# Kernel tuning notes

Measured on AMD Instinct MI355X. Metric: run time of the kernel, lower is better.

The kernel has to match this reference:

```python
import jax, jax.numpy as jnp
import numpy as np

B, S, D, H, E = 4, 1024, 1024, 16, 4
HD = D // H
FF = 4 * D
EPS = 1e-5


def _ln(x):
    # normalize only; per-expert affine applied by caller
    mu = jnp.mean(x, axis=-1, keepdims=True)
    var = jnp.mean(jnp.square(x - mu), axis=-1, keepdims=True)
    return (x - mu) * jax.lax.rsqrt(var + EPS)


def setup_inputs() -> dict:
    key = jax.random.key(0)
    ks = jax.random.split(key, 12)
    s = 0.02
    inp = {
        "x": jax.random.normal(ks[0], (B, S, D), jnp.float32),
        # attention router
        "Wr_a": jax.random.normal(ks[1], (D, E), jnp.float32) * s,
        "br_a": jnp.zeros((E,), jnp.float32),
        # per-expert attention params
        "g_a": jnp.ones((E, D), jnp.float32),
        "b_a": jnp.zeros((E, D), jnp.float32),
        "Wqkv": jax.random.normal(ks[2], (E, D, 3 * D), jnp.float32) * s,
        "bqkv": jnp.zeros((E, 3 * D), jnp.float32),
        "Wpr": jax.random.normal(ks[3], (E, D, D), jnp.float32) * s,
        "bpr": jnp.zeros((E, D), jnp.float32),
        # MLP router
        "Wr_m": jax.random.normal(ks[4], (D, E), jnp.float32) * s,
        "br_m": jnp.zeros((E,), jnp.float32),
        # per-expert MLP params
        "g_m": jnp.ones((E, D), jnp.float32),
        "b_m": jnp.zeros((E, D), jnp.float32),
        "Wfc": jax.random.normal(ks[5], (E, D, FF), jnp.float32) * s,
        "bfc": jnp.zeros((E, FF), jnp.float32),
        "Wp2": jax.random.normal(ks[6], (E, FF, D), jnp.float32) * s,
        "bp2": jnp.zeros((E, D), jnp.float32),
    }
    return inp


def _block(x, Wr_a, br_a, g_a, b_a, Wqkv, bqkv, Wpr, bpr,
           Wr_m, br_m, g_m, b_m, Wfc, bfc, Wp2, bp2):
    N = B * S
    h = x.reshape(N, D)

    # ---- MoT attention (routing_all_possible_path: dense score-weighted mix) ----
    score = jax.nn.softmax(h @ Wr_a + br_a, axis=-1)          # [N,E]
    hn = _ln(h)                                                # shared normalization
    hln = hn[None, :, :] * g_a[:, None, :] + b_a[:, None, :]  # [E,N,D]
    qkv_e = jnp.einsum('end,edf->enf', hln, Wqkv) + bqkv[:, None, :]  # [E,N,3D]
    qkv = jnp.einsum('ne,enf->nf', score, qkv_e)               # [N,3D]

    q, k, v = jnp.split(qkv.reshape(B, S, 3 * D), 3, axis=-1)
    q = q.reshape(B, S, H, HD).transpose(0, 2, 1, 3)           # [B,H,S,hd]
    k = k.reshape(B, S, H, HD).transpose(0, 2, 1, 3)
    v = v.reshape(B, S, H, HD).transpose(0, 2, 1, 3)

    aw = jnp.einsum('bhqd,bhkd->bhqk', q, k) / jnp.sqrt(jnp.float32(HD))
    causal = jnp.tril(jnp.ones((S, S), bool))
    aw = jnp.where(causal, aw, jnp.finfo(aw.dtype).min)
    p = jax.nn.softmax(aw, axis=-1)
    a = jnp.einsum('bhqk,bhkd->bhqd', p, v)                    # [B,H,S,hd]
    a = a.transpose(0, 2, 1, 3).reshape(N, D)

    attn_out = jnp.einsum('ne,nd,edf->nf', score, a, Wpr) + score @ bpr
    y = x + attn_out.reshape(B, S, D)

    # ---- MoT MLP (same dense routed-expert pattern) ----
    h2 = y.reshape(N, D)
    score2 = jax.nn.softmax(h2 @ Wr_m + br_m, axis=-1)         # [N,E]
    hn2 = _ln(h2)
    hln2 = hn2[None, :, :] * g_m[:, None, :] + b_m[:, None, :]  # [E,N,D]
    inter = jax.nn.gelu(jnp.einsum('end,edf->enf', hln2, Wfc) + bfc[:, None, :])  # [E,N,FF]
    mlp_out = jnp.einsum('ne,enf,efd->nd', score2, inter, Wp2) + score2 @ bp2
    return y + mlp_out.reshape(B, S, D)


def reference(x, Wr_a, br_a, g_a, b_a, Wqkv, bqkv, Wpr, bpr,
              Wr_m, br_m, g_m, b_m, Wfc, bfc, Wp2, bp2):
    return _block(x, Wr_a, br_a, g_a, b_a, Wqkv, bqkv, Wpr, bpr,
                  Wr_m, br_m, g_m, b_m, Wfc, bfc, Wp2, bp2)
```

## Files before the change

kernel.cpp:

```cpp
#include <hip/hip_runtime.h>
#include <hip/hip_bf16.h>

typedef __bf16 bf16x8 __attribute__((ext_vector_type(8)));
typedef float f32x4 __attribute__((ext_vector_type(4)));
typedef unsigned short u16;
typedef u16 u16x8 __attribute__((ext_vector_type(8)));

#define B_ 4
#define S_ 1024
#define D_ 1024
#define E_ 4
#define H_ 16
#define FF_ 4096
#define N_ 4096

__device__ __forceinline__ u16 f2bf(float f) {
  __hip_bfloat16 h = __float2bfloat16(f);
  return *reinterpret_cast<u16*>(&h);
}
__device__ __forceinline__ float bf2f(u16 v) {
  return __uint_as_float(((unsigned)v) << 16);
}

#define BAR()                         \
  {                                   \
    asm volatile("" ::: "memory");    \
    __builtin_amdgcn_s_barrier();     \
    asm volatile("" ::: "memory");    \
  }

__global__ __launch_bounds__(256) void tcvt(const float* __restrict__ src,
                                            u16* __restrict__ dst, int R, int C) {
  __shared__ float t[32][33];
  int r0 = blockIdx.y * 32, c0 = blockIdx.x * 32;
  int tx = threadIdx.x, ty = threadIdx.y;
#pragma unroll
  for (int i = 0; i < 4; i++)
    t[ty + i * 8][tx] = src[(long)(r0 + ty + i * 8) * C + c0 + tx];
  __syncthreads();
#pragma unroll
  for (int i = 0; i < 4; i++)
    dst[(long)(c0 + ty + i * 8) * R + r0 + tx] = f2bf(t[tx][ty + i * 8]);
}

template <int YMODE>
__global__ __launch_bounds__(256) void ln_router_expand(
    const float* __restrict__ X, const float* __restrict__ Wr, const float* __restrict__ br,
    const float* __restrict__ g, const float* __restrict__ bb,
    float* __restrict__ score_out, u16* __restrict__ Aout,
    long stride_e, long stride_n, int scale_flag,
    const float* __restrict__ score_a, const float* __restrict__ bpr,
    const u16* __restrict__ prt, float* __restrict__ ybuf) {
  int n = blockIdx.x, t = threadIdx.x;
  int lane = t & 63, wave = t >> 6;
  const float* xr = X + (long)n * D_;
  float xv[4];
  float vals[6] = {0.f, 0.f, 0.f, 0.f, 0.f, 0.f};
  float4 sa4;
  if (YMODE) sa4 = reinterpret_cast<const float4*>(score_a)[n];
#pragma unroll
  for (int i = 0; i < 4; i++) {
    int d = i * 256 + t;
    float v = xr[d];
    if (YMODE) {
      long idx = (long)n * D_ + d;
      v += sa4.x * bpr[d] + sa4.y * bpr[D_ + d] + sa4.z * bpr[2 * D_ + d] +
           sa4.w * bpr[3 * D_ + d];
#pragma unroll
      for (int zz = 0; zz < 4; zz++) v += bf2f(prt[(long)zz * 4194304 + idx]);
      ybuf[idx] = v;
    }
    xv[i] = v;
    vals[0] += v;
    vals[1] += v * v;
    float4 w = reinterpret_cast<const float4*>(Wr)[d];
    vals[2] += v * w.x; vals[3] += v * w.y; vals[4] += v * w.z; vals[5] += v * w.w;
  }
#pragma unroll
  for (int o = 1; o < 64; o <<= 1) {
#pragma unroll
    for (int j = 0; j < 6; j++) vals[j] += __shfl_xor(vals[j], o, 64);
  }
  __shared__ float red[4][6];
  if (lane == 0) {
#pragma unroll
    for (int j = 0; j < 6; j++) red[wave][j] = vals[j];
  }
  __syncthreads();
  float tot[6];
#pragma unroll
  for (int j = 0; j < 6; j++) tot[j] = red[0][j] + red[1][j] + red[2][j] + red[3][j];
  float mean = tot[0] * (1.0f / D_);
  float var = tot[1] * (1.0f / D_) - mean * mean;
  float rstd = rsqrtf(var + 1e-5f);
  float lg0 = tot[2] + br[0], lg1 = tot[3] + br[1], lg2 = tot[4] + br[2], lg3 = tot[5] + br[3];
  float mx = fmaxf(fmaxf(lg0, lg1), fmaxf(lg2, lg3));
  float e0 = __expf(lg0 - mx), e1 = __expf(lg1 - mx), e2 = __expf(lg2 - mx), e3 = __expf(lg3 - mx);
  float inv = 1.0f / (e0 + e1 + e2 + e3);
  float sc[4] = {e0 * inv, e1 * inv, e2 * inv, e3 * inv};
  if (t == 0) {
    float4 s4 = make_float4(sc[0], sc[1], sc[2], sc[3]);
    *reinterpret_cast<float4*>(&score_out[(long)n * 4]) = s4;
  }
#pragma unroll
  for (int i = 0; i < 4; i++) {
    int d = i * 256 + t;
    float hn = (xv[i] - mean) * rstd;
#pragma unroll
    for (int e = 0; e < 4; e++) {
      float val = hn * g[e * D_ + d] + bb[e * D_ + d];
      if (scale_flag) val *= sc[e];
      Aout[(long)e * stride_e + (long)n * stride_n + d] = f2bf(val);
    }
  }
}

template <int MODE>
__global__ __launch_bounds__(512, 2) void g8(
    const u16* __restrict__ A, const u16* __restrict__ Bt, int K, int N, int kslice,
    const float* __restrict__ score, const float* __restrict__ bias,
    u16* __restrict__ outb, int eidx, long zstride) {
  __shared__ __align__(16) u16 lds0[65536];
  const int tid = threadIdx.x;
  const int w = tid >> 6, lane = tid & 63;
  const int l15 = lane & 15, l4 = lane >> 4;
  const int wr = w >> 2, wc = w & 3;

  const int gx = gridDim.x, gy = gridDim.y;
  const int total = gx * gy * gridDim.z;
  const int flat = blockIdx.x + gx * (blockIdx.y + gy * blockIdx.z);
  const int cpx = total >> 3;
  const int nf = (flat & 7) * cpx + (flat >> 3);
  const int bxi = nf % gx;
  const int tmp = nf / gx;
  const int byi = tmp % gy;
  const int z = tmp / gy;

  const long bm = (long)byi * 256, bn = (long)bxi * 256;
  const long k0 = (long)z * kslice;
  const int nt = kslice >> 6;

  const int cp = lane & 3;
  const int sr0 = w * 32 + (lane >> 2);
  const int sr1 = sr0 + 16;
  const int cl0 = cp ^ ((sr0 >> 1) & 3);
  const int cl1 = cp ^ ((sr1 >> 1) & 3);
  const u16* gA0 = A + (bm + sr0) * (long)K + k0 + cl0 * 8;
  const u16* gA1 = A + (bm + sr1) * (long)K + k0 + cl1 * 8;
  const u16* gB0 = Bt + (bn + sr0) * (long)K + k0 + cl0 * 8;
  const u16* gB1 = Bt + (bn + sr1) * (long)K + k0 + cl1 * 8;
  const int e0 = w * 1024;
  const int e1 = w * 1024 + 512;

  const int chA = l4 ^ ((l15 >> 1) & 3);
  const int rdA = (wr * 128 + l15) * 32 + chA * 8;
  const int rdB = (wc * 64 + l15) * 32 + chA * 8;

#define GLD(gsrc, ldsoff)                                                              \
  __builtin_amdgcn_global_load_lds(                                                    \
      (const __attribute__((address_space(1))) void*)(gsrc),                           \
      (__attribute__((address_space(3))) void*)(lds0 + (ldsoff)), 16, 0, 0)

  GLD(gA0, 0 + e0);
  GLD(gA1, 0 + e1);
  GLD(gB0, 16384 + e0);
  GLD(gB1, 16384 + e1);
  GLD(gA0 + 32, 8192 + e0);
  GLD(gA1 + 32, 8192 + e1);
  GLD(gB0 + 32, 24576 + e0);
  GLD(gB1 + 32, 24576 + e1);
  if (nt > 1) {
    GLD(gA0 + 64, 32768 + e0);
    GLD(gA1 + 64, 32768 + e1);
    GLD(gB0 + 64, 32768 + 16384 + e0);
    GLD(gB1 + 64, 32768 + 16384 + e1);
    asm volatile("s_waitcnt vmcnt(8)" ::: "memory");
  } else {
    asm volatile("s_waitcnt vmcnt(4)" ::: "memory");
  }
  BAR();

  f32x4 acc[8][4] = {};
  bf16x8 a[4], b[4];

  for (int t = 0; t < nt; ++t) {
    const int base = (t & 1) * 32768;
    const int nb = base ^ 32768;
    const long ko1 = (long)(t + 1) * 64 + 32;
    const long ko2 = (long)(t + 2) * 64;
#pragma unroll
    for (int i = 0; i < 4; i++) a[i] = *(const bf16x8*)(lds0 + base + rdA + i * 512);
#pragma unroll
    for (int i = 0; i < 4; i++) b[i] = *(const bf16x8*)(lds0 + base + 16384 + rdB + i * 512);
    if (t + 1 < nt) {
      GLD(gA0 + ko1, nb + 8192 + e0);
      GLD(gA1 + ko1, nb + 8192 + e1);
    }
    BAR();
    __builtin_amdgcn_s_setprio(1);
#pragma unroll
    for (int mi = 0; mi < 4; mi++)
#pragma unroll
      for (int ni = 0; ni < 4; ni++)
        acc[mi][ni] = __builtin_amdgcn_mfma_f32_16x16x32_bf16(a[mi], b[ni], acc[mi][ni], 0, 0, 0);
    __builtin_amdgcn_s_setprio(0);
    BAR();
#pragma unroll
    for (int i = 0; i < 4; i++) a[i] = *(const bf16x8*)(lds0 + base + rdA + (4 + i) * 512);
    if (t + 1 < nt) {
      GLD(gB0 + ko1, nb + 24576 + e0);
      GLD(gB1 + ko1, nb + 24576 + e1);
    }
    BAR();
    __builtin_amdgcn_s_setprio(1);
#pragma unroll
    for (int mi = 0; mi < 4; mi++)
#pragma unroll
      for (int ni = 0; ni < 4; ni++)
        acc[4 + mi][ni] =
            __builtin_amdgcn_mfma_f32_16x16x32_bf16(a[mi], b[ni], acc[4 + mi][ni], 0, 0, 0);
    __builtin_amdgcn_s_setprio(0);
    if (t + 1 < nt) {
      asm volatile("s_waitcnt vmcnt(8)" ::: "memory");
    } else {
      asm volatile("s_waitcnt vmcnt(0)" ::: "memory");
    }
    BAR();
#pragma unroll
    for (int i = 0; i < 4; i++) a[i] = *(const bf16x8*)(lds0 + base + 8192 + rdA + i * 512);
#pragma unroll
    for (int i = 0; i < 4; i++) b[i] = *(const bf16x8*)(lds0 + base + 24576 + rdB + i * 512);
    if (t + 2 < nt) {
      GLD(gA0 + ko2, base + e0);
      GLD(gA1 + ko2, base + e1);
    }
    BAR();
    __builtin_amdgcn_s_setprio(1);
#pragma unroll
    for (int mi = 0; mi < 4; mi++)
#pragma unroll
      for (int ni = 0; ni < 4; ni++)
        acc[mi][ni] = __builtin_amdgcn_mfma_f32_16x16x32_bf16(a[mi], b[ni], acc[mi][ni], 0, 0, 0);
    __builtin_amdgcn_s_setprio(0);
    BAR();
#pragma unroll
    for (int i = 0; i < 4; i++)
      a[i] = *(const bf16x8*)(lds0 + base + 8192 + rdA + (4 + i) * 512);
    if (t + 2 < nt) {
      GLD(gB0 + ko2, base + 16384 + e0);
      GLD(gB1 + ko2, base + 16384 + e1);
    }
    BAR();
    __builtin_amdgcn_s_setprio(1);
#pragma unroll
    for (int mi = 0; mi < 4; mi++)
#pragma unroll
      for (int ni = 0; ni < 4; ni++)
        acc[4 + mi][ni] =
            __builtin_amdgcn_mfma_f32_16x16x32_bf16(a[mi], b[ni], acc[4 + mi][ni], 0, 0, 0);
    __builtin_amdgcn_s_setprio(0);
    if (t + 2 < nt) {
      asm volatile("s_waitcnt vmcnt(8)" ::: "memory");
    } else if (t + 1 < nt) {
      asm volatile("s_waitcnt vmcnt(4)" ::: "memory");
    } else {
      asm volatile("s_waitcnt vmcnt(0)" ::: "memory");
    }
    BAR();
  }
#undef GLD

  const long zoff = (long)z * zstride;
#pragma unroll
  for (int ni = 0; ni < 4; ni++) {
    long col = bn + wc * 64 + ni * 16 + l15;
    float b4[4];
    float bcol = 0.0f;
    if (MODE == 0) {
#pragma unroll
      for (int e = 0; e < 4; e++) b4[e] = bias[(long)e * N + col];
    } else if (MODE == 2) {
      bcol = bias[col];
    }
#pragma unroll
    for (int mi = 0; mi < 8; mi++) {
#pragma unroll
      for (int r = 0; r < 4; r++) {
        long row = bm + wr * 128 + mi * 16 + l4 * 4 + r;
        float v = acc[mi][ni][r];
        if (MODE == 0) {
          float4 s4 = reinterpret_cast<const float4*>(score)[row];
          v += s4.x * b4[0] + s4.y * b4[1] + s4.z * b4[2] + s4.w * b4[3];
          outb[row * (long)N + col] = f2bf(v);
        } else if (MODE == 2) {
          float u = v + bcol;
          float zz = 0.7978845608f * (u + 0.044715f * u * u * u);
          float tt = __expf(2.0f * zz);
          float gel = u * (1.0f - 1.0f / (tt + 1.0f));
          outb[row * (long)N + col] = f2bf(gel * score[row * 4 + eidx]);
        } else {
          outb[zoff + row * (long)N + col] = f2bf(v);
        }
      }
    }
  }
}

__global__ __launch_bounds__(256) void attn_kernel(const u16* __restrict__ qkv,
                                                   const float* __restrict__ score_a,
                                                   u16* __restrict__ A_pr) {
  __shared__ __align__(16) u16 Kt[32 * 64];
  __shared__ __align__(16) u16 VT[64 * 32];
  __shared__ __align__(16) u16 Pl[4][16 * 32];
  int tid = threadIdx.x, wave = tid >> 6, lane = tid & 63;
  int l15 = lane & 15, l4 = lane >> 4;
  int qblk = blockIdx.x, bh = blockIdx.y;
  int b = bh >> 4, h = bh & 15;
  int q0 = qblk * 64 + wave * 16;
  const long LD = 3072;

  bf16x8 qf[2];
  {
    const u16* qp = qkv + (long)(b * 1024 + q0 + l15) * LD + h * 64 + l4 * 8;
    qf[0] = *(const bf16x8*)qp;
    qf[1] = *(const bf16x8*)(qp + 32);
  }
  f32x4 acc[4] = {};
  float m_run = -1e30f, l_run = 0.0f;
  int kv_end = qblk * 64 + 64;

  for (int kv0 = 0; kv0 < kv_end; kv0 += 32) {
    {
      int r = tid >> 3, c = (tid & 7) * 8;
      const u16* kp = qkv + (long)(b * 1024 + kv0 + r) * LD + 1024 + h * 64 + c;
      *(u16x8*)&Kt[r * 64 + c] = *(const u16x8*)kp;
      u16x8 vv = *(const u16x8*)(kp + 1024);
#pragma unroll
      for (int j = 0; j < 8; j++) VT[(c + j) * 32 + r] = vv[j];
    }
    __syncthreads();
    if (kv0 < q0 + 16) {
      float p[8];
      float pmax = -1e30f;
      int qg = q0 + l15;
#pragma unroll
      for (int ks = 0; ks < 2; ks++) {
        f32x4 st = {};
#pragma unroll
        for (int kc = 0; kc < 2; kc++) {
          bf16x8 kf = *(const bf16x8*)&Kt[(ks * 16 + l15) * 64 + kc * 32 + l4 * 8];
          st = __builtin_amdgcn_mfma_f32_16x16x32_bf16(kf, qf[kc], st, 0, 0, 0);
        }
#pragma unroll
        for (int r = 0; r < 4; r++) {
          int kvg = kv0 + ks * 16 + l4 * 4 + r;
          float v = st[r] * 0.125f;
          if (kvg > qg) v = -1e30f;
          p[ks * 4 + r] = v;
          pmax = fmaxf(pmax, v);
        }
      }
      pmax = fmaxf(pmax, __shfl_xor(pmax, 16, 64));
      pmax = fmaxf(pmax, __shfl_xor(pmax, 32, 64));
      float m_new = fmaxf(m_run, pmax);
      float alpha = __expf(m_run - m_new);
      float rsum = 0.f;
#pragma unroll
      for (int i = 0; i < 8; i++) {
        p[i] = __expf(p[i] - m_new);
        rsum += p[i];
      }
      rsum += __shfl_xor(rsum, 16, 64);
      rsum += __shfl_xor(rsum, 32, 64);
      l_run = l_run * alpha + rsum;
      m_run = m_new;
      float af4[4];
#pragma unroll
      for (int r = 0; r < 4; r++) af4[r] = __shfl(alpha, l4 * 4 + r, 64);
#pragma unroll
      for (int i = 0; i < 4; i++) {
#pragma unroll
        for (int r = 0; r < 4; r++) acc[i][r] *= af4[r];
      }
      u16* pw = &Pl[wave][0];
#pragma unroll
      for (int i = 0; i < 8; i++) {
        int ks = i >> 2, r = i & 3;
        pw[l15 * 32 + ks * 16 + l4 * 4 + r] = f2bf(p[i]);
      }
      bf16x8 pa = *(const bf16x8*)&pw[l15 * 32 + l4 * 8];
#pragma unroll
      for (int i = 0; i < 4; i++) {
        bf16x8 vf = *(const bf16x8*)&VT[(i * 16 + l15) * 32 + l4 * 8];
        acc[i] = __builtin_amdgcn_mfma_f32_16x16x32_bf16(pa, vf, acc[i], 0, 0, 0);
      }
    }
    __syncthreads();
  }

  float linv[4];
#pragma unroll
  for (int r = 0; r < 4; r++) {
    float lv = __shfl(l_run, l4 * 4 + r, 64);
    linv[r] = 1.0f / lv;
  }
#pragma unroll
  for (int r = 0; r < 4; r++) {
    int q = l4 * 4 + r;
    long nrow = (long)b * 1024 + q0 + q;
    float4 s4 = reinterpret_cast<const float4*>(score_a)[nrow];
    float se[4] = {s4.x, s4.y, s4.z, s4.w};
#pragma unroll
    for (int i = 0; i < 4; i++) {
      float v = acc[i][r] * linv[r];
      int d = h * 64 + i * 16 + l15;
#pragma unroll
      for (int e = 0; e < 4; e++) A_pr[nrow * 4096 + e * 1024 + d] = f2bf(se[e] * v);
    }
  }
}

template <int FIRST>
__global__ __launch_bounds__(256) void accum_out(const float* __restrict__ ybuf,
                                                 const float* __restrict__ score_m,
                                                 const float* __restrict__ bp2,
                                                 const u16* __restrict__ p2t,
                                                 float* __restrict__ out) {
  int n = blockIdx.x, t = threadIdx.x;
#pragma unroll
  for (int i = 0; i < 4; i++) {
    int d = i * 256 + t;
    long idx = (long)n * D_ + d;
    float v;
    if (FIRST) {
      float4 s4 = reinterpret_cast<const float4*>(score_m)[n];
      v = ybuf[idx] + s4.x * bp2[d] + s4.y * bp2[D_ + d] + s4.z * bp2[2 * D_ + d] +
          s4.w * bp2[3 * D_ + d];
    } else {
      v = out[idx];
    }
#pragma unroll
    for (int zz = 0; zz < 4; zz++) v += bf2f(p2t[(long)zz * 4194304 + idx]);
    out[idx] = v;
  }
}

extern "C" void kernel_launch(void* const* d_in, const int* in_sizes, int n_in, void* d_out,
                              int out_size, void* d_ws, size_t ws_size, hipStream_t stream) {
  (void)in_sizes; (void)n_in; (void)out_size; (void)ws_size;
  const float* x    = (const float*)d_in[0];
  const float* Wr_a = (const float*)d_in[1];
  const float* br_a = (const float*)d_in[2];
  const float* g_a  = (const float*)d_in[3];
  const float* b_a  = (const float*)d_in[4];
  const float* Wqkv = (const float*)d_in[5];
  const float* bqkv = (const float*)d_in[6];
  const float* Wpr  = (const float*)d_in[7];
  const float* bpr  = (const float*)d_in[8];
  const float* Wr_m = (const float*)d_in[9];
  const float* br_m = (const float*)d_in[10];
  const float* g_m  = (const float*)d_in[11];
  const float* b_m  = (const float*)d_in[12];
  const float* Wfc  = (const float*)d_in[13];
  const float* bfc  = (const float*)d_in[14];
  const float* Wp2  = (const float*)d_in[15];
  const float* bp2  = (const float*)d_in[16];
  float* out = (float*)d_out;

  char* ws = (char*)d_ws;
  const size_t oW = 0;
  const size_t oA = 25165824;
  const size_t oQ = oA + 33554432;
  const size_t oP = oQ + 33554432;
  const size_t oY = oP + 33554432;
  const size_t oS = oY + 16777216;
  u16* wt_qkv  = (u16*)(ws + oW);
  u16* wt_pr   = (u16*)(ws + oW);
  u16* wt_fce  = (u16*)(ws + oW);
  u16* wt_p2e  = (u16*)(ws + oW + (size_t)8 * 1024 * 1024);
  u16* A_a     = (u16*)(ws + oA);
  u16* prt     = (u16*)(ws + oA);
  u16* A_fc    = (u16*)(ws + oA);
  u16* qkvb    = (u16*)(ws + oQ);
  u16* p2t     = (u16*)(ws + oQ);
  u16* A_pr    = (u16*)(ws + oP);
  u16* inter   = (u16*)(ws + oP);
  float* ybuf  = (float*)(ws + oY);
  float* score_a = (float*)(ws + oS);
  float* score_m = (float*)(ws + oS + 65536);

  dim3 tb(32, 8);
  tcvt<<<dim3(3072 / 32, 4096 / 32), tb, 0, stream>>>(Wqkv, wt_qkv, 4096, 3072);
  ln_router_expand<0><<<N_, 256, 0, stream>>>(x, Wr_a, br_a, g_a, b_a, score_a, A_a,
                                              (long)1024, (long)4096, 1,
                                              nullptr, nullptr, nullptr, nullptr);
  g8<0><<<dim3(3072 / 256, 4096 / 256, 1), 512, 0, stream>>>(
      A_a, wt_qkv, 4096, 3072, 4096, score_a, bqkv, qkvb, 0, 0L);
  attn_kernel<<<dim3(S_ / 64, B_ * H_), 256, 0, stream>>>(qkvb, score_a, A_pr);
  tcvt<<<dim3(1024 / 32, 4096 / 32), tb, 0, stream>>>(Wpr, wt_pr, 4096, 1024);
  g8<4><<<dim3(1024 / 256, 4096 / 256, 4), 512, 0, stream>>>(
      A_pr, wt_pr, 4096, 1024, 1024, nullptr, nullptr, prt, 0, (long)4096 * 1024);

  ln_router_expand<1><<<N_, 256, 0, stream>>>(x, Wr_m, br_m, g_m, b_m,
                                              score_m, A_fc, (long)N_ * 1024, (long)1024, 0,
                                              score_a, bpr, prt, ybuf);
  for (int e = 0; e < 4; e++) {
    tcvt<<<dim3(4096 / 32, 1024 / 32), tb, 0, stream>>>(
        Wfc + (size_t)e * 1024 * 4096, wt_fce, 1024, 4096);
    g8<2><<<dim3(4096 / 256, 4096 / 256, 1), 512, 0, stream>>>(
        A_fc + (size_t)e * N_ * 1024, wt_fce, 1024, 4096, 1024, score_m,
        bfc + e * 4096, inter, e, 0L);
    tcvt<<<dim3(1024 / 32, 4096 / 32), tb, 0, stream>>>(
        Wp2 + (size_t)e * 4096 * 1024, wt_p2e, 4096, 1024);
    g8<4><<<dim3(1024 / 256, 4096 / 256, 4), 512, 0, stream>>>(
        inter, wt_p2e, 4096, 1024, 1024, nullptr, nullptr, p2t, 0, (long)4096 * 1024);
    if (e == 0) {
      accum_out<1><<<N_, 256, 0, stream>>>(ybuf, score_m, bp2, p2t, out);
    } else {
      accum_out<0><<<N_, 256, 0, stream>>>(nullptr, nullptr, nullptr, p2t, out);
    }
  }
}
```

Measured before the change: 804.2 us.

## Merge GEMM half-tile MFMA phases and vectorize elementwise LN/accumulate kernels

The main GEMM loop now loads all 8 A fragments at once and issues 32 MFMAs per k-half instead of two 16-MFMA phases. This removes half the barriers per iteration and issues both A and B prefetch loads together. The LN/router and output-accumulate kernels switch from strided scalar loads to float4/u16x4 vector loads, with each thread handling 4 contiguous elements. The risks are higher register pressure from the 8 A fragments under launch_bounds(512,2), and less interleaving of global loads with compute.

```diff
diff --git a/kernel.cpp b/kernel.cpp
--- a/kernel.cpp
+++ b/kernel.cpp
@@ -5,6 +5,7 @@
 typedef float f32x4 __attribute__((ext_vector_type(4)));
 typedef unsigned short u16;
 typedef u16 u16x8 __attribute__((ext_vector_type(8)));
+typedef u16 u16x4 __attribute__((ext_vector_type(4)));
 
 #define B_ 4
 #define S_ 1024
@@ -53,28 +54,39 @@
     const u16* __restrict__ prt, float* __restrict__ ybuf) {
   int n = blockIdx.x, t = threadIdx.x;
   int lane = t & 63, wave = t >> 6;
+  int d0 = t * 4;
   const float* xr = X + (long)n * D_;
-  float xv[4];
-  float vals[6] = {0.f, 0.f, 0.f, 0.f, 0.f, 0.f};
-  float4 sa4;
-  if (YMODE) sa4 = reinterpret_cast<const float4*>(score_a)[n];
-#pragma unroll
-  for (int i = 0; i < 4; i++) {
-    int d = i * 256 + t;
-    float v = xr[d];
-    if (YMODE) {
-      long idx = (long)n * D_ + d;
-      v += sa4.x * bpr[d] + sa4.y * bpr[D_ + d] + sa4.z * bpr[2 * D_ + d] +
-           sa4.w * bpr[3 * D_ + d];
-#pragma unroll
-      for (int zz = 0; zz < 4; zz++) v += bf2f(prt[(long)zz * 4194304 + idx]);
-      ybuf[idx] = v;
-    }
-    xv[i] = v;
-    vals[0] += v;
-    vals[1] += v * v;
-    float4 w = reinterpret_cast<const float4*>(Wr)[d];
-    vals[2] += v * w.x; vals[3] += v * w.y; vals[4] += v * w.z; vals[5] += v * w.w;
+  float4 xv = *reinterpret_cast<const float4*>(&xr[d0]);
+  if (YMODE) {
+    float4 sa4 = reinterpret_cast<const float4*>(score_a)[n];
+    float4 b0 = *reinterpret_cast<const float4*>(&bpr[d0]);
+    float4 b1 = *reinterpret_cast<const float4*>(&bpr[D_ + d0]);
+    float4 b2 = *reinterpret_cast<const float4*>(&bpr[2 * D_ + d0]);
+    float4 b3 = *reinterpret_cast<const float4*>(&bpr[3 * D_ + d0]);
+    xv.x += sa4.x * b0.x + sa4.y * b1.x + sa4.z * b2.x + sa4.w * b3.x;
+    xv.y += sa4.x * b0.y + sa4.y * b1.y + sa4.z * b2.y + sa4.w * b3.y;
+    xv.z += sa4.x * b0.z + sa4.y * b1.z + sa4.z * b2.z + sa4.w * b3.z;
+    xv.w += sa4.x * b0.w + sa4.y * b1.w + sa4.z * b2.w + sa4.w * b3.w;
+    long idx = (long)n * D_ + d0;
+#pragma unroll
+    for (int zz = 0; zz < 4; zz++) {
+      u16x4 pv = *reinterpret_cast<const u16x4*>(&prt[(long)zz * 4194304 + idx]);
+      xv.x += bf2f(pv[0]); xv.y += bf2f(pv[1]); xv.z += bf2f(pv[2]); xv.w += bf2f(pv[3]);
+    }
+    *reinterpret_cast<float4*>(&ybuf[idx]) = xv;
+  }
+  float vals[6];
+  vals[0] = xv.x + xv.y + xv.z + xv.w;
+  vals[1] = xv.x * xv.x + xv.y * xv.y + xv.z * xv.z + xv.w * xv.w;
+  {
+    float4 w0 = reinterpret_cast<const float4*>(Wr)[d0];
+    float4 w1 = reinterpret_cast<const float4*>(Wr)[d0 + 1];
+    float4 w2 = reinterpret_cast<const float4*>(Wr)[d0 + 2];
+    float4 w3 = reinterpret_cast<const float4*>(Wr)[d0 + 3];
+    vals[2] = xv.x * w0.x + xv.y * w1.x + xv.z * w2.x + xv.w * w3.x;
+    vals[3] = xv.x * w0.y + xv.y * w1.y + xv.z * w2.y + xv.w * w3.y;
+    vals[4] = xv.x * w0.z + xv.y * w1.z + xv.z * w2.z + xv.w * w3.z;
+    vals[5] = xv.x * w0.w + xv.y * w1.w + xv.z * w2.w + xv.w * w3.w;
   }
 #pragma unroll
   for (int o = 1; o < 64; o <<= 1) {
@@ -102,16 +114,20 @@
     float4 s4 = make_float4(sc[0], sc[1], sc[2], sc[3]);
     *reinterpret_cast<float4*>(&score_out[(long)n * 4]) = s4;
   }
-#pragma unroll
-  for (int i = 0; i < 4; i++) {
-    int d = i * 256 + t;
-    float hn = (xv[i] - mean) * rstd;
-#pragma unroll
-    for (int e = 0; e < 4; e++) {
-      float val = hn * g[e * D_ + d] + bb[e * D_ + d];
-      if (scale_flag) val *= sc[e];
-      Aout[(long)e * stride_e + (long)n * stride_n + d] = f2bf(val);
-    }
+  float4 hn;
+  hn.x = (xv.x - mean) * rstd; hn.y = (xv.y - mean) * rstd;
+  hn.z = (xv.z - mean) * rstd; hn.w = (xv.w - mean) * rstd;
+#pragma unroll
+  for (int e = 0; e < 4; e++) {
+    float4 ge = *reinterpret_cast<const float4*>(&g[e * D_ + d0]);
+    float4 be = *reinterpret_cast<const float4*>(&bb[e * D_ + d0]);
+    float s = scale_flag ? sc[e] : 1.0f;
+    u16x4 o;
+    o[0] = f2bf((hn.x * ge.x + be.x) * s);
+    o[1] = f2bf((hn.y * ge.y + be.y) * s);
+    o[2] = f2bf((hn.z * ge.z + be.z) * s);
+    o[3] = f2bf((hn.w * ge.w + be.w) * s);
+    *reinterpret_cast<u16x4*>(&Aout[(long)e * stride_e + (long)n * stride_n + d0]) = o;
   }
 }
 
@@ -181,7 +197,7 @@
   BAR();
 
   f32x4 acc[8][4] = {};
-  bf16x8 a[4], b[4];
+  bf16x8 a[8], b[4];
 
   for (int t = 0; t < nt; ++t) {
     const int base = (t & 1) * 32768;
@@ -189,36 +205,22 @@
     const long ko1 = (long)(t + 1) * 64 + 32;
     const long ko2 = (long)(t + 2) * 64;
 #pragma unroll
-    for (int i = 0; i < 4; i++) a[i] = *(const bf16x8*)(lds0 + base + rdA + i * 512);
+    for (int i = 0; i < 8; i++) a[i] = *(const bf16x8*)(lds0 + base + rdA + i * 512);
 #pragma unroll
     for (int i = 0; i < 4; i++) b[i] = *(const bf16x8*)(lds0 + base + 16384 + rdB + i * 512);
     if (t + 1 < nt) {
       GLD(gA0 + ko1, nb + 8192 + e0);
       GLD(gA1 + ko1, nb + 8192 + e1);
+      GLD(gB0 + ko1, nb + 24576 + e0);
+      GLD(gB1 + ko1, nb + 24576 + e1);
     }
     BAR();
     __builtin_amdgcn_s_setprio(1);
 #pragma unroll
-    for (int mi = 0; mi < 4; mi++)
+    for (int mi = 0; mi < 8; mi++)
 #pragma unroll
       for (int ni = 0; ni < 4; ni++)
         acc[mi][ni] = __builtin_amdgcn_mfma_f32_16x16x32_bf16(a[mi], b[ni], acc[mi][ni], 0, 0, 0);
-    __builtin_amdgcn_s_setprio(0);
-    BAR();
-#pragma unroll
-    for (int i = 0; i < 4; i++) a[i] = *(const bf16x8*)(lds0 + base + rdA + (4 + i) * 512);
-    if (t + 1 < nt) {
-      GLD(gB0 + ko1, nb + 24576 + e0);
-      GLD(gB1 + ko1, nb + 24576 + e1);
-    }
-    BAR();
-    __builtin_amdgcn_s_setprio(1);
-#pragma unroll
-    for (int mi = 0; mi < 4; mi++)
-#pragma unroll
-      for (int ni = 0; ni < 4; ni++)
-        acc[4 + mi][ni] =
-            __builtin_amdgcn_mfma_f32_16x16x32_bf16(a[mi], b[ni], acc[4 + mi][ni], 0, 0, 0);
     __builtin_amdgcn_s_setprio(0);
     if (t + 1 < nt) {
       asm volatile("s_waitcnt vmcnt(8)" ::: "memory");
@@ -227,37 +229,22 @@
     }
     BAR();
 #pragma unroll
-    for (int i = 0; i < 4; i++) a[i] = *(const bf16x8*)(lds0 + base + 8192 + rdA + i * 512);
+    for (int i = 0; i < 8; i++) a[i] = *(const bf16x8*)(lds0 + base + 8192 + rdA + i * 512);
 #pragma unroll
     for (int i = 0; i < 4; i++) b[i] = *(const bf16x8*)(lds0 + base + 24576 + rdB + i * 512);
     if (t + 2 < nt) {
       GLD(gA0 + ko2, base + e0);
       GLD(gA1 + ko2, base + e1);
+      GLD(gB0 + ko2, base + 16384 + e0);
+      GLD(gB1 + ko2, base + 16384 + e1);
     }
     BAR();
     __builtin_amdgcn_s_setprio(1);
 #pragma unroll
-    for (int mi = 0; mi < 4; mi++)
+    for (int mi = 0; mi < 8; mi++)
 #pragma unroll
       for (int ni = 0; ni < 4; ni++)
         acc[mi][ni] = __builtin_amdgcn_mfma_f32_16x16x32_bf16(a[mi], b[ni], acc[mi][ni], 0, 0, 0);
-    __builtin_amdgcn_s_setprio(0);
-    BAR();
-#pragma unroll
-    for (int i = 0; i < 4; i++)
-      a[i] = *(const bf16x8*)(lds0 + base + 8192 + rdA + (4 + i) * 512);
-    if (t + 2 < nt) {
-      GLD(gB0 + ko2, base + 16384 + e0);
-      GLD(gB1 + ko2, base + 16384 + e1);
-    }
-    BAR();
-    __builtin_amdgcn_s_setprio(1);
-#pragma unroll
-    for (int mi = 0; mi < 4; mi++)
-#pragma unroll
-      for (int ni = 0; ni < 4; ni++)
-        acc[4 + mi][ni] =
-            __builtin_amdgcn_mfma_f32_16x16x32_bf16(a[mi], b[ni], acc[4 + mi][ni], 0, 0, 0);
     __builtin_amdgcn_s_setprio(0);
     if (t + 2 < nt) {
       asm volatile("s_waitcnt vmcnt(8)" ::: "memory");
@@ -427,22 +414,29 @@
                                                  const u16* __restrict__ p2t,
                                                  float* __restrict__ out) {
   int n = blockIdx.x, t = threadIdx.x;
-#pragma unroll
-  for (int i = 0; i < 4; i++) {
-    int d = i * 256 + t;
-    long idx = (long)n * D_ + d;
-    float v;
-    if (FIRST) {
-      float4 s4 = reinterpret_cast<const float4*>(score_m)[n];
-      v = ybuf[idx] + s4.x * bp2[d] + s4.y * bp2[D_ + d] + s4.z * bp2[2 * D_ + d] +
-          s4.w * bp2[3 * D_ + d];
-    } else {
-      v = out[idx];
-    }
-#pragma unroll
-    for (int zz = 0; zz < 4; zz++) v += bf2f(p2t[(long)zz * 4194304 + idx]);
-    out[idx] = v;
-  }
+  int d0 = t * 4;
+  long idx = (long)n * D_ + d0;
+  float4 v;
+  if (FIRST) {
+    float4 s4 = reinterpret_cast<const float4*>(score_m)[n];
+    float4 b0 = *reinterpret_cast<const float4*>(&bp2[d0]);
+    float4 b1 = *reinterpret_cast<const float4*>(&bp2[D_ + d0]);
+    float4 b2 = *reinterpret_cast<const float4*>(&bp2[2 * D_ + d0]);
+    float4 b3 = *reinterpret_cast<const float4*>(&bp2[3 * D_ + d0]);
+    v = *reinterpret_cast<const float4*>(&ybuf[idx]);
+    v.x += s4.x * b0.x + s4.y * b1.x + s4.z * b2.x + s4.w * b3.x;
+    v.y += s4.x * b0.y + s4.y * b1.y + s4.z * b2.y + s4.w * b3.y;
+    v.z += s4.x * b0.z + s4.y * b1.z + s4.z * b2.z + s4.w * b3.z;
+    v.w += s4.x * b0.w + s4.y * b1.w + s4.z * b2.w + s4.w * b3.w;
+  } else {
+    v = *reinterpret_cast<const float4*>(&out[idx]);
+  }
+#pragma unroll
+  for (int zz = 0; zz < 4; zz++) {
+    u16x4 pv = *reinterpret_cast<const u16x4*>(&p2t[(long)zz * 4194304 + idx]);
+    v.x += bf2f(pv[0]); v.y += bf2f(pv[1]); v.z += bf2f(pv[2]); v.w += bf2f(pv[3]);
+  }
+  *reinterpret_cast<float4*>(&out[idx]) = v;
 }
 
 extern "C" void kernel_launch(void* const* d_in, const int* in_sizes, int n_in, void* d_out,
```

Result: no change. 800.3 us (-0.5%).
